# Optimization experiments

Measured on AMD Instinct MI355X. Metric: run time of the kernel, lower is better.

Reference implementation:

```python
import jax, jax.numpy as jnp
import numpy as np

S, B, L = 512, 256, 128  # sent_len, batch, label_num
START_ID = 126


def setup_inputs() -> dict:
    key = jax.random.key(0)
    k1, k2, k3 = jax.random.split(key, 3)
    emit_scores = jax.random.normal(k1, (S, B, L), dtype=jnp.float32)
    T = jax.random.normal(k2, (L, L), dtype=jnp.float32) * 0.1  # transition[prev, cur]
    labels = jax.random.randint(k3, (B, S), 0, START_ID)  # gold tags, excluding START
    return {"emit_scores": emit_scores, "T": T, "labels": labels, "start_id": START_ID}


def _crf_loss(emit_scores, T, labels, start_id):
    S_, B_, L_ = emit_scores.shape
    # ---- gold path score: sum_t emit[t,b,y_t] + T[y_{t-1}, y_t], y_{-1}=START ----
    prev = jnp.concatenate(
        [jnp.full((B_, 1), start_id, dtype=labels.dtype), labels[:, :-1]], axis=1
    )  # (B,S)
    cur = labels  # (B,S)
    # emit_scores[t, b, cur[b, t]] -> (S,B)
    emit_gold = jnp.take_along_axis(
        emit_scores, cur.T[:, :, None], axis=2
    )[:, :, 0]
    gold = jnp.sum(emit_gold) + jnp.sum(T[prev, cur])
    # ---- partition via forward algorithm (log-semiring scan) ----
    # Faithful to crf_encoder: fwd_0 = emit[0] (no START transition at t=0).
    def step(fwd, emit_t):
        # fwd: (B, L) over prev label i; new[b,j] = LSE_i(fwd[b,i] + T[i,j]) + emit_t[b,j]
        fwd_new = jax.nn.logsumexp(fwd[:, :, None] + T[None, :, :], axis=1) + emit_t
        return fwd_new, None

    fwd_final, _ = jax.lax.scan(step, emit_scores[0], emit_scores[1:])
    log_z = jnp.sum(jax.nn.logsumexp(fwd_final, axis=1))
    return log_z - gold


def reference(emit_scores, T, labels, start_id):
    return _crf_loss(emit_scores, T, labels, start_id)
```

## Files before the change

### kernel.cpp

```cpp
#include <hip/hip_runtime.h>


#define LOG2E 1.4426950408889634f
#define LN2F  0.6931471805599453f

typedef float        f32x4  __attribute__((ext_vector_type(4)));
typedef int          i32x8  __attribute__((ext_vector_type(8)));
typedef unsigned int u32x4  __attribute__((ext_vector_type(4)));
typedef short        bf16x8 __attribute__((ext_vector_type(8)));
typedef __bf16       bf16x2 __attribute__((ext_vector_type(2)));

__device__ __forceinline__ unsigned packbf2(float lo, float hi) {
    bf16x2 p = { (__bf16)lo, (__bf16)hi };
    return __builtin_bit_cast(unsigned, p);
}

#define MFMAX(Aop, Bop, SCL) \
    __builtin_amdgcn_mfma_scale_f32_16x16x128_f8f6f4( \
        Aop, Bop, zero4, 0, 1, 0, 0x7F7F7F7F, 0, SCL)

__global__ __launch_bounds__(64) void crf_setup_kernel(
    const float* __restrict__ Tm, int* __restrict__ Afrbuf)
{
    const int dir = blockIdx.x >> 3;
    const int jt  = blockIdx.x & 7;
    const int l   = threadIdx.x;
    const int b   = l & 15;
    const int g   = l >> 4;
    i32x8 af;
#pragma unroll
    for (int d = 0; d < 8; ++d) {
        float a0, a1, a2, a3;
        if (!dir) {
            const int rb = 16 * d + 4 * g, col = 16 * jt + b;
            a0 = __builtin_amdgcn_exp2f(Tm[(rb + 0) * 128 + col] * LOG2E);
            a1 = __builtin_amdgcn_exp2f(Tm[(rb + 1) * 128 + col] * LOG2E);
            a2 = __builtin_amdgcn_exp2f(Tm[(rb + 2) * 128 + col] * LOG2E);
            a3 = __builtin_amdgcn_exp2f(Tm[(rb + 3) * 128 + col] * LOG2E);
        } else {
            const int row = 16 * jt + b, cb = 16 * d + 4 * g;
            a0 = __builtin_amdgcn_exp2f(Tm[row * 128 + cb + 0] * LOG2E);
            a1 = __builtin_amdgcn_exp2f(Tm[row * 128 + cb + 1] * LOG2E);
            a2 = __builtin_amdgcn_exp2f(Tm[row * 128 + cb + 2] * LOG2E);
            a3 = __builtin_amdgcn_exp2f(Tm[row * 128 + cb + 3] * LOG2E);
        }
        int w = __builtin_amdgcn_cvt_pk_fp8_f32(a0, a1, 0, false);
        af[d] = __builtin_amdgcn_cvt_pk_fp8_f32(a2, a3, w, true);
    }
    *(i32x8*)&Afrbuf[((size_t)blockIdx.x * 64 + l) * 8] = af;
}

__global__ __launch_bounds__(256, 2) void crf_chunk_kernel(
    const float* __restrict__ emit,
    const int*   __restrict__ Afrbuf,
    float* __restrict__ yx,
    int*   __restrict__ Ls)
{
    const int bi    = blockIdx.x;
    const int chunk = bi >> 4;
    const int gb    = bi & 15;
    const int tid   = threadIdx.x;
    const int NT    = (chunk == 63) ? 7 : 8;
    const int t0    = 1 + 8 * chunk;

    __shared__ __align__(16) float xt[16384];

#pragma unroll
    for (int i = 0; i < 16; ++i) {
        const int f4 = i * 256 + tid;
        const int r  = f4 >> 5;
        const int c  = f4 & 31;
        const int k  = r >> 4;
        const int bb = r & 15;
        int t = t0 + k; if (t > 511) t = 511;
        const float4 e = *(const float4*)(emit
            + (size_t)t * 32768 + (gb * 16 + bb) * 128 + 4 * c);
        f32x4 o;
        o[0] = __builtin_amdgcn_exp2f(e.x * LOG2E);
        o[1] = __builtin_amdgcn_exp2f(e.y * LOG2E);
        o[2] = __builtin_amdgcn_exp2f(e.z * LOG2E);
        o[3] = __builtin_amdgcn_exp2f(e.w * LOG2E);
        *(f32x4*)&xt[r * 128 + 4 * (c ^ (bb & 7))] = o;
    }
    __syncthreads();

    const int wv = tid >> 6;
    if (wv >= 2) return;

    const int dir = wv;
    const int l   = tid & 63;
    const int b   = l & 15;
    const int g   = l >> 4;
    const int bg  = gb * 16 + b;
    const int bsw = b & 7;
    const f32x4 zero4 = {0.f, 0.f, 0.f, 0.f};

    i32x8 Afr[8];
#pragma unroll
    for (int jt = 0; jt < 8; ++jt)
        Afr[jt] = *(const i32x8*)&Afrbuf[(((size_t)dir * 8 + jt) * 64 + l) * 8];

    i32x8 Bq;
    f32x4 u[8];
    int L, sclw;
    if (!dir) {
        int one2 = __builtin_amdgcn_cvt_pk_bf8_f32(1.f, 1.f, 0, false);
        one2 = __builtin_amdgcn_cvt_pk_bf8_f32(1.f, 1.f, one2, true);
#pragma unroll
        for (int d = 0; d < 8; ++d) Bq[d] = one2;
        L = 4;  sclw = 123 * 0x01010101;
    } else {
#pragma unroll
        for (int d = 0; d < 8; ++d) u[d] = (f32x4){1.f, 1.f, 1.f, 1.f};
        L = 8;  sclw = 119 * 0x01010101;
    }

    const size_t obase = ((size_t)(bg * 2 + dir) * 64 + chunk) * 128;

#pragma unroll
    for (int k = 0; k < 8; ++k) {
        if (k < NT) {
            const int krow = dir ? (NT - 1 - k) : k;
            f32x4 xv[8];
#pragma unroll
            for (int jt = 0; jt < 8; ++jt)
                xv[jt] = *(const f32x4*)&xt[(krow * 16 + b) * 128
                                            + 4 * ((4 * jt + g) ^ bsw)];
            if (dir) {
#pragma unroll
                for (int d = 0; d < 8; ++d) {
                    f32x4 w = xv[d] * u[d];
                    int bw = __builtin_amdgcn_cvt_pk_bf8_f32(w[0], w[1], 0, false);
                    Bq[d]  = __builtin_amdgcn_cvt_pk_bf8_f32(w[2], w[3], bw, true);
                }
            }
            f32x4 ac[8];
#pragma unroll
            for (int jt = 0; jt < 8; ++jt)
                ac[jt] = MFMAX(Afr[jt], Bq, sclw);
            float a00 = __shfl(ac[0][0], b);
            int ea = (__float_as_int(a00) >> 23) & 0xFF;
            int sb = (dir ? 248 : 250) - ea;
            sb = sb < 1 ? 1 : (sb > 254 ? 254 : sb);
            const bool last = (k == NT - 1);
            if (!last) { L += 127 - sb; sclw = sb * 0x01010101; }
            if (!dir) {
#pragma unroll
                for (int jt = 0; jt < 8; ++jt) {
                    f32x4 vv = ac[jt] * xv[jt];
                    if (last) *(f32x4*)&yx[obase + 16 * jt + 4 * g] = vv;
                    else {
                        int bw = __builtin_amdgcn_cvt_pk_bf8_f32(vv[0], vv[1], 0, false);
                        Bq[jt] = __builtin_amdgcn_cvt_pk_bf8_f32(vv[2], vv[3], bw, true);
                    }
                }
            } else {
#pragma unroll
                for (int jt = 0; jt < 8; ++jt) {
                    u[jt] = ac[jt];
                    if (last) *(f32x4*)&yx[obase + 16 * jt + 4 * g] = ac[jt];
                }
            }
        }
    }
    if (l < 16)
        Ls[((gb * 16 + l) * 2 + dir) * 64 + chunk] = L;
}

__global__ __launch_bounds__(256) void crf_dots_kernel(
    const float* __restrict__ emit, const float* __restrict__ yx,
    const int* __restrict__ Ls, float* __restrict__ scan_part)
{
    const int b = blockIdx.x;
    const int w = threadIdx.x >> 6;
    const int l = threadIdx.x & 63;
    __shared__ float r[4];

    const float* yb  = yx + (size_t)(b * 2) * 64 * 128;
    const float* xb  = yb + 64 * 128;
    const int*   Lyb = Ls + b * 2 * 64;

    float acc = 0.f;
#pragma unroll 1
    for (int c = w; c <= 64; c += 4) {
        float term;
        if (c == 64) {
            const float* yp = yb + 63 * 128;
            float s = yp[l] + yp[64 + l];
#pragma unroll
            for (int off = 1; off < 64; off <<= 1) s += __shfl_xor(s, off);
            term = __log2f(s) + (float)Lyb[63];
        } else {
            float pa, pb;
            if (c == 0) {
                pa = __builtin_amdgcn_exp2f(emit[b * 128 + l] * LOG2E);
                pb = __builtin_amdgcn_exp2f(emit[b * 128 + 64 + l] * LOG2E);
            } else {
                const float* yp = yb + (c - 1) * 128;
                pa = yp[l]; pb = yp[64 + l];
            }
            const float* xp = xb + c * 128;
            float xa = xp[l], xb2 = xp[64 + l];
            float sp = pa * xa + pb * xb2;
            float tp = xa + xb2;
#pragma unroll
            for (int off = 1; off < 64; off <<= 1) {
                sp += __shfl_xor(sp, off);
                tp += __shfl_xor(tp, off);
            }
            term = __log2f(sp) - __log2f(tp)
                 + (c ? (float)Lyb[c - 1] : 0.f);
        }
        acc += term;
    }
    if (l == 0) r[w] = acc;
    __syncthreads();
    if (threadIdx.x == 0)
        scan_part[b] = ((r[0] + r[1]) + (r[2] + r[3])) * LN2F;
}

#define MFMAB(Aop, Bop, Cop) \
    __builtin_amdgcn_mfma_f32_16x16x32_bf16( \
        __builtin_bit_cast(bf16x8, Aop), __builtin_bit_cast(bf16x8, Bop), Cop, 0, 0, 0)

#define STEPB(SLOT, TPF, DOPF, RN, LAST) do {                                 \
    f32x4 ac[8];                                                              \
    _Pragma("unroll") for (int jt = 0; jt < 8; ++jt)                          \
        ac[jt] = MFMAB(Afr[0][jt], Bf[0], zero4);                             \
    _Pragma("unroll") for (int ch = 1; ch < 4; ++ch)                          \
        _Pragma("unroll") for (int jt = 0; jt < 8; ++jt)                      \
            ac[jt] = MFMAB(Afr[ch][jt], Bf[ch], ac[jt]);                      \
    float xv[8][4];                                                           \
    _Pragma("unroll") for (int jt = 0; jt < 8; ++jt) {                        \
        float4 xw = xbf[SLOT][jt];                                            \
        xv[jt][0] = __builtin_amdgcn_exp2f(xw.x * LOG2E);                     \
        xv[jt][1] = __builtin_amdgcn_exp2f(xw.y * LOG2E);                     \
        xv[jt][2] = __builtin_amdgcn_exp2f(xw.z * LOG2E);                     \
        xv[jt][3] = __builtin_amdgcn_exp2f(xw.w * LOG2E);                     \
    }                                                                         \
    if (DOPF) {                                                               \
        int tp = (TPF); if (tp > 511) tp = 511;                               \
        _Pragma("unroll") for (int jt = 0; jt < 8; ++jt)                      \
            xbf[SLOT][jt] = emf4[8192 * tp + lb + 4 * jt];                    \
    }                                                                         \
    float vv[8][4];                                                           \
    _Pragma("unroll") for (int jt = 0; jt < 8; ++jt)                          \
        _Pragma("unroll") for (int r = 0; r < 4; ++r)                         \
            vv[jt][r] = ac[jt][r] * xv[jt][r];                                \
    if (RN) {                                                                 \
        float mx = vv[0][0];                                                  \
        _Pragma("unroll") for (int jt = 0; jt < 8; ++jt)                      \
            _Pragma("unroll") for (int r = 0; r < 4; ++r)                     \
                mx = fmaxf(mx, vv[jt][r]);                                    \
        mx = fmaxf(mx, __shfl_xor(mx, 16));                                   \
        mx = fmaxf(mx, __shfl_xor(mx, 32));                                   \
        int Ee = (__float_as_int(mx) >> 23) & 0xFF;                           \
        if (Ee > 254) Ee = 254;                                               \
        ls2 += Ee - 127;                                                      \
        float scl = __int_as_float((254 - Ee) << 23);                         \
        _Pragma("unroll") for (int jt = 0; jt < 8; ++jt)                      \
            _Pragma("unroll") for (int r = 0; r < 4; ++r)                     \
                vv[jt][r] *= scl;                                             \
    }                                                                         \
    if (LAST) {                                                               \
        fin = 0.f;                                                            \
        _Pragma("unroll") for (int jt = 0; jt < 8; ++jt)                      \
            fin += (vv[jt][0] + vv[jt][1]) + (vv[jt][2] + vv[jt][3]);         \
    } else {                                                                  \
        _Pragma("unroll") for (int ch = 0; ch < 4; ++ch) {                    \
            Bf[ch][0] = packbf2(vv[2*ch][0],     vv[2*ch][1]);                \
            Bf[ch][1] = packbf2(vv[2*ch][2],     vv[2*ch][3]);                \
            Bf[ch][2] = packbf2(vv[2*ch + 1][0], vv[2*ch + 1][1]);            \
            Bf[ch][3] = packbf2(vv[2*ch + 1][2], vv[2*ch + 1][3]);            \
        }                                                                     \
    }                                                                         \
} while (0)

__global__ __launch_bounds__(64, 1) void crf_scan_bf16_kernel(
    const float* __restrict__ emit,
    const float* __restrict__ Tm,
    float* __restrict__ scan_part)
{
    const int gb = blockIdx.x;
    const int l  = threadIdx.x;
    const int b  = l & 15;
    const int g  = l >> 4;
    const int bg = gb * 16 + b;
    const int lb = 32 * bg + g;

    const float4* emf4 = (const float4*)emit;
    const f32x4 zero4 = {0.f, 0.f, 0.f, 0.f};

    u32x4 Afr[4][8];
#pragma unroll
    for (int ch = 0; ch < 4; ++ch)
#pragma unroll
        for (int p = 0; p < 4; ++p) {
            const int e0 = 2 * p, e1 = 2 * p + 1;
            const int jp0 = 32 * ch + 16 * (e0 >> 2) + 4 * g + (e0 & 3);
            const int jp1 = 32 * ch + 16 * (e1 >> 2) + 4 * g + (e1 & 3);
#pragma unroll
            for (int jt = 0; jt < 8; ++jt) {
                float a0 = __builtin_amdgcn_exp2f(Tm[jp0 * 128 + 16 * jt + b] * LOG2E);
                float a1 = __builtin_amdgcn_exp2f(Tm[jp1 * 128 + 16 * jt + b] * LOG2E);
                Afr[ch][jt][p] = packbf2(a0, a1);
            }
        }

    u32x4 Bf[4];
    {
        float x0[8][4];
#pragma unroll
        for (int jt = 0; jt < 8; ++jt) {
            float4 e = emf4[lb + 4 * jt];
            x0[jt][0] = __builtin_amdgcn_exp2f(e.x * LOG2E);
            x0[jt][1] = __builtin_amdgcn_exp2f(e.y * LOG2E);
            x0[jt][2] = __builtin_amdgcn_exp2f(e.z * LOG2E);
            x0[jt][3] = __builtin_amdgcn_exp2f(e.w * LOG2E);
        }
#pragma unroll
        for (int ch = 0; ch < 4; ++ch) {
            Bf[ch][0] = packbf2(x0[2 * ch][0],     x0[2 * ch][1]);
            Bf[ch][1] = packbf2(x0[2 * ch][2],     x0[2 * ch][3]);
            Bf[ch][2] = packbf2(x0[2 * ch + 1][0], x0[2 * ch + 1][1]);
            Bf[ch][3] = packbf2(x0[2 * ch + 1][2], x0[2 * ch + 1][3]);
        }
    }

    float4 xbf[4][8];
#pragma unroll
    for (int k = 0; k < 4; ++k)
#pragma unroll
        for (int jt = 0; jt < 8; ++jt)
            xbf[k][jt] = emf4[8192 * (1 + k) + lb + 4 * jt];

    int ls2 = 0;
    float fin = 0.f;

#pragma unroll 1
    for (int grp = 0; grp < 63; ++grp) {
        const int t0 = 1 + 8 * grp;
        STEPB(0, t0 + 4,  1, 0, 0);
        STEPB(1, t0 + 5,  1, 0, 0);
        STEPB(2, t0 + 6,  1, 0, 0);
        STEPB(3, t0 + 7,  1, 0, 0);
        STEPB(0, t0 + 8,  1, 0, 0);
        STEPB(1, t0 + 9,  1, 0, 0);
        STEPB(2, t0 + 10, 1, 0, 0);
        STEPB(3, t0 + 11, 1, 1, 0);
    }
    STEPB(0, 509, 1, 0, 0);
    STEPB(1, 510, 1, 0, 0);
    STEPB(2, 511, 1, 0, 0);
    STEPB(3, 0,   0, 0, 0);
    STEPB(0, 0,   0, 0, 0);
    STEPB(1, 0,   0, 0, 0);
    STEPB(2, 0,   0, 0, 1);

    fin += __shfl_xor(fin, 16);
    fin += __shfl_xor(fin, 32);
    if (l < 16)
        scan_part[gb * 16 + l] = ((float)ls2 + __log2f(fin)) * LN2F;
}

__global__ __launch_bounds__(256) void crf_gold_kernel(
    const float* __restrict__ emit, const float* __restrict__ Tm,
    const int* __restrict__ labels, const int* __restrict__ startp,
    float* __restrict__ gold_part)
{
    const int b = blockIdx.x, tid = threadIdx.x;
    __shared__ int lab[512];
    __shared__ float r[4];
    lab[tid]       = labels[b * 512 + tid];
    lab[tid + 256] = labels[b * 512 + tid + 256];
    __syncthreads();
    float s = 0.f;
    {
        int y0 = lab[tid];
        int p0 = (tid == 0) ? startp[0] : lab[tid - 1];
        s += emit[((size_t)tid * 256 + b) * 128 + y0] + Tm[p0 * 128 + y0];
        int t1 = tid + 256;
        int y1 = lab[t1];
        int p1 = lab[t1 - 1];
        s += emit[((size_t)t1 * 256 + b) * 128 + y1] + Tm[p1 * 128 + y1];
    }
#pragma unroll
    for (int off = 1; off < 64; off <<= 1) s += __shfl_xor(s, off);
    if ((tid & 63) == 0) r[tid >> 6] = s;
    __syncthreads();
    if (tid == 0) gold_part[b] = (r[0] + r[1]) + (r[2] + r[3]);
}

__global__ __launch_bounds__(256) void crf_final_kernel(
    const float* __restrict__ scan_part, const float* __restrict__ gold_part,
    float* __restrict__ out)
{
    const int tid = threadIdx.x;
    __shared__ float r[4];
    float v = scan_part[tid] - gold_part[tid];
#pragma unroll
    for (int off = 1; off < 64; off <<= 1) v += __shfl_xor(v, off);
    if ((tid & 63) == 0) r[tid >> 6] = v;
    __syncthreads();
    if (tid == 0) out[0] = (r[0] + r[1]) + (r[2] + r[3]);
}

extern "C" void kernel_launch(void* const* d_in, const int* in_sizes, int n_in,
                              void* d_out, int out_size, void* d_ws, size_t ws_size,
                              hipStream_t stream) {
    const float* emit   = (const float*)d_in[0];
    const float* Tm     = (const float*)d_in[1];
    const int*   labels = (const int*)d_in[2];
    const int*   startp = (const int*)d_in[3];

    const size_t af_bytes = (size_t)2 * 8 * 64 * 32;
    const size_t yx_bytes = (size_t)256 * 2 * 64 * 128 * 4;
    const size_t Ls_bytes = (size_t)256 * 2 * 64 * 4;

    if (ws_size >= af_bytes + yx_bytes + Ls_bytes + 4096) {
        int*   Afrbuf    = (int*)d_ws;
        float* yx        = (float*)((char*)d_ws + af_bytes);
        int*   Ls        = (int*)((char*)d_ws + af_bytes + yx_bytes);
        float* scan_part = (float*)((char*)d_ws + af_bytes + yx_bytes + Ls_bytes);
        float* gold_part = scan_part + 256;
        crf_setup_kernel<<<16,   64, 0, stream>>>(Tm, Afrbuf);
        crf_chunk_kernel<<<1024, 256, 0, stream>>>(emit, Afrbuf, yx, Ls);
        crf_gold_kernel <<<256, 256, 0, stream>>>(emit, Tm, labels, startp, gold_part);
        crf_dots_kernel <<<256, 256, 0, stream>>>(emit, yx, Ls, scan_part);
        crf_final_kernel<<<1,   256, 0, stream>>>(scan_part, gold_part, (float*)d_out);
    } else {
        float* scan_part = (float*)d_ws;
        float* gold_part = scan_part + 256;
        crf_scan_bf16_kernel<<<16, 64, 0, stream>>>(emit, Tm, scan_part);
        crf_gold_kernel<<<256, 256, 0, stream>>>(emit, Tm, labels, startp, gold_part);
        crf_final_kernel<<<1, 256, 0, stream>>>(scan_part, gold_part, (float*)d_out);
    }
}
```

Measured before the change: 52.23 us.

## Store exp(emit) tile as bf16 in LDS and fuse gold into dots kernel

The chunk kernel now stores exponentiated emissions in shared memory as bf16 instead of fp32. This halves LDS use and allows launch_bounds occupancy 4 instead of 2. The gold-path score is folded into the dots kernel, and the final reduction becomes a small sum kernel, so one launch is dropped. The cost is extra bf16 rounding on the emission factors before they are quantized to bf8 anyway, which carries a small accuracy risk.

```diff
diff --git a/kernel.cpp b/kernel.cpp
--- a/kernel.cpp
+++ b/kernel.cpp
@@ -14,6 +14,8 @@
     bf16x2 p = { (__bf16)lo, (__bf16)hi };
     return __builtin_bit_cast(unsigned, p);
 }
+__device__ __forceinline__ float bflo(unsigned w) { return __uint_as_float(w << 16); }
+__device__ __forceinline__ float bfhi(unsigned w) { return __uint_as_float(w & 0xFFFF0000u); }
 
 #define MFMAX(Aop, Bop, SCL) \
     __builtin_amdgcn_mfma_scale_f32_16x16x128_f8f6f4( \
@@ -50,7 +52,7 @@
     *(i32x8*)&Afrbuf[((size_t)blockIdx.x * 64 + l) * 8] = af;
 }
 
-__global__ __launch_bounds__(256, 2) void crf_chunk_kernel(
+__global__ __launch_bounds__(256, 4) void crf_chunk_kernel(
     const float* __restrict__ emit,
     const int*   __restrict__ Afrbuf,
     float* __restrict__ yx,
@@ -63,24 +65,29 @@
     const int NT    = (chunk == 63) ? 7 : 8;
     const int t0    = 1 + 8 * chunk;
 
-    __shared__ __align__(16) float xt[16384];
-
-#pragma unroll
-    for (int i = 0; i < 16; ++i) {
-        const int f4 = i * 256 + tid;
-        const int r  = f4 >> 5;
-        const int c  = f4 & 31;
-        const int k  = r >> 4;
-        const int bb = r & 15;
+    __shared__ __align__(16) unsigned short xt[16384];
+
+#pragma unroll
+    for (int i = 0; i < 8; ++i) {
+        const int lin = i * 256 + tid;
+        const int r   = lin >> 4;
+        const int c16 = lin & 15;
+        const int k   = r >> 4;
+        const int bb  = r & 15;
         int t = t0 + k; if (t > 511) t = 511;
-        const float4 e = *(const float4*)(emit
-            + (size_t)t * 32768 + (gb * 16 + bb) * 128 + 4 * c);
-        f32x4 o;
-        o[0] = __builtin_amdgcn_exp2f(e.x * LOG2E);
-        o[1] = __builtin_amdgcn_exp2f(e.y * LOG2E);
-        o[2] = __builtin_amdgcn_exp2f(e.z * LOG2E);
-        o[3] = __builtin_amdgcn_exp2f(e.w * LOG2E);
-        *(f32x4*)&xt[r * 128 + 4 * (c ^ (bb & 7))] = o;
+        const float4* gp = (const float4*)(emit + (size_t)t * 32768
+                                           + (gb * 16 + bb) * 128 + 8 * c16);
+        const float4 e0 = gp[0], e1 = gp[1];
+        u32x4 o;
+        o[0] = packbf2(__builtin_amdgcn_exp2f(e0.x * LOG2E),
+                       __builtin_amdgcn_exp2f(e0.y * LOG2E));
+        o[1] = packbf2(__builtin_amdgcn_exp2f(e0.z * LOG2E),
+                       __builtin_amdgcn_exp2f(e0.w * LOG2E));
+        o[2] = packbf2(__builtin_amdgcn_exp2f(e1.x * LOG2E),
+                       __builtin_amdgcn_exp2f(e1.y * LOG2E));
+        o[3] = packbf2(__builtin_amdgcn_exp2f(e1.z * LOG2E),
+                       __builtin_amdgcn_exp2f(e1.w * LOG2E));
+        *(u32x4*)&xt[r * 128 + ((c16 ^ (bb & 7)) << 3)] = o;
     }
     __syncthreads();
 
@@ -123,9 +130,13 @@
             const int krow = dir ? (NT - 1 - k) : k;
             f32x4 xv[8];
 #pragma unroll
-            for (int jt = 0; jt < 8; ++jt)
-                xv[jt] = *(const f32x4*)&xt[(krow * 16 + b) * 128
-                                            + 4 * ((4 * jt + g) ^ bsw)];
+            for (int jt = 0; jt < 8; ++jt) {
+                const int c16r = 2 * jt + (g >> 1);
+                const uint2 uu = *(const uint2*)&xt[(krow * 16 + b) * 128
+                    + ((c16r ^ bsw) << 3) + (g & 1) * 4];
+                xv[jt][0] = bflo(uu.x); xv[jt][1] = bfhi(uu.x);
+                xv[jt][2] = bflo(uu.y); xv[jt][3] = bfhi(uu.y);
+            }
             if (dir) {
 #pragma unroll
                 for (int d = 0; d < 8; ++d) {
@@ -167,14 +178,36 @@
         Ls[((gb * 16 + l) * 2 + dir) * 64 + chunk] = L;
 }
 
-__global__ __launch_bounds__(256) void crf_dots_kernel(
+__global__ __launch_bounds__(256) void crf_dotsgold_kernel(
     const float* __restrict__ emit, const float* __restrict__ yx,
-    const int* __restrict__ Ls, float* __restrict__ scan_part)
-{
-    const int b = blockIdx.x;
-    const int w = threadIdx.x >> 6;
-    const int l = threadIdx.x & 63;
-    __shared__ float r[4];
+    const int* __restrict__ Ls, const float* __restrict__ Tm,
+    const int* __restrict__ labels, const int* __restrict__ startp,
+    float* __restrict__ diff_part)
+{
+    const int b   = blockIdx.x;
+    const int tid = threadIdx.x;
+    const int w   = tid >> 6;
+    const int l   = tid & 63;
+    __shared__ int lab[512];
+    __shared__ float rg[4], rd[4];
+
+    lab[tid]       = labels[b * 512 + tid];
+    lab[tid + 256] = labels[b * 512 + tid + 256];
+    __syncthreads();
+
+    float s = 0.f;
+    {
+        int y0 = lab[tid];
+        int p0 = (tid == 0) ? startp[0] : lab[tid - 1];
+        s += emit[((size_t)tid * 256 + b) * 128 + y0] + Tm[p0 * 128 + y0];
+        int t1 = tid + 256;
+        int y1 = lab[t1];
+        int p1 = lab[t1 - 1];
+        s += emit[((size_t)t1 * 256 + b) * 128 + y1] + Tm[p1 * 128 + y1];
+    }
+#pragma unroll
+    for (int off = 1; off < 64; off <<= 1) s += __shfl_xor(s, off);
+    if (l == 0) rg[w] = s;
 
     const float* yb  = yx + (size_t)(b * 2) * 64 * 128;
     const float* xb  = yb + 64 * 128;
@@ -186,10 +219,10 @@
         float term;
         if (c == 64) {
             const float* yp = yb + 63 * 128;
-            float s = yp[l] + yp[64 + l];
-#pragma unroll
-            for (int off = 1; off < 64; off <<= 1) s += __shfl_xor(s, off);
-            term = __log2f(s) + (float)Lyb[63];
+            float s2 = yp[l] + yp[64 + l];
+#pragma unroll
+            for (int off = 1; off < 64; off <<= 1) s2 += __shfl_xor(s2, off);
+            term = __log2f(s2) + (float)Lyb[63];
         } else {
             float pa, pb;
             if (c == 0) {
@@ -213,10 +246,26 @@
         }
         acc += term;
     }
-    if (l == 0) r[w] = acc;
-    __syncthreads();
-    if (threadIdx.x == 0)
-        scan_part[b] = ((r[0] + r[1]) + (r[2] + r[3])) * LN2F;
+    if (l == 0) rd[w] = acc;
+    __syncthreads();
+    if (tid == 0) {
+        float lz   = ((rd[0] + rd[1]) + (rd[2] + rd[3])) * LN2F;
+        float gold = (rg[0] + rg[1]) + (rg[2] + rg[3]);
+        diff_part[b] = lz - gold;
+    }
+}
+
+__global__ __launch_bounds__(256) void crf_sum_kernel(
+    const float* __restrict__ diff_part, float* __restrict__ out)
+{
+    const int tid = threadIdx.x;
+    __shared__ float r[4];
+    float v = diff_part[tid];
+#pragma unroll
+    for (int off = 1; off < 64; off <<= 1) v += __shfl_xor(v, off);
+    if ((tid & 63) == 0) r[tid >> 6] = v;
+    __syncthreads();
+    if (tid == 0) out[0] = (r[0] + r[1]) + (r[2] + r[3]);
 }
 
 #define MFMAB(Aop, Bop, Cop) \
@@ -421,13 +470,12 @@
         int*   Afrbuf    = (int*)d_ws;
         float* yx        = (float*)((char*)d_ws + af_bytes);
         int*   Ls        = (int*)((char*)d_ws + af_bytes + yx_bytes);
-        float* scan_part = (float*)((char*)d_ws + af_bytes + yx_bytes + Ls_bytes);
-        float* gold_part = scan_part + 256;
-        crf_setup_kernel<<<16,   64, 0, stream>>>(Tm, Afrbuf);
-        crf_chunk_kernel<<<1024, 256, 0, stream>>>(emit, Afrbuf, yx, Ls);
-        crf_gold_kernel <<<256, 256, 0, stream>>>(emit, Tm, labels, startp, gold_part);
-        crf_dots_kernel <<<256, 256, 0, stream>>>(emit, yx, Ls, scan_part);
-        crf_final_kernel<<<1,   256, 0, stream>>>(scan_part, gold_part, (float*)d_out);
+        float* diff_part = (float*)((char*)d_ws + af_bytes + yx_bytes + Ls_bytes);
+        crf_setup_kernel   <<<16,   64, 0, stream>>>(Tm, Afrbuf);
+        crf_chunk_kernel   <<<1024, 256, 0, stream>>>(emit, Afrbuf, yx, Ls);
+        crf_dotsgold_kernel<<<256,  256, 0, stream>>>(emit, yx, Ls, Tm, labels,
+                                                      startp, diff_part);
+        crf_sum_kernel     <<<1,    256, 0, stream>>>(diff_part, (float*)d_out);
     } else {
         float* scan_part = (float*)d_ws;
         float* gold_part = scan_part + 256;
```

Measured after the change: 89.18 us. +70.8%, slower.
